# Kernel optimization log

Hardware: AMD Instinct MI355X
Metric: run time of the kernel (lower is better)

Reference implementation:

```python
import jax, jax.numpy as jnp
import numpy as np

B, S, D = 2, 2048, 512
WIN = 64  # local causal window (includes current token)
EPS = 1e-5


def setup_inputs() -> dict:
    key = jax.random.key(0)
    ks = jax.random.split(key, 8)
    sc = 0.02
    return {
        "x":  jax.random.normal(ks[0], (B, S, D), jnp.float32),
        "Wq": jax.random.normal(ks[1], (D, D), jnp.float32) * sc,
        "bq": jnp.zeros((D,), jnp.float32),
        "Wk": jax.random.normal(ks[2], (D, D), jnp.float32) * sc,
        "bk": jnp.zeros((D,), jnp.float32),
        "Wv": jax.random.normal(ks[3], (D, D), jnp.float32) * sc,
        "bv": jnp.zeros((D,), jnp.float32),
        "Wo": jax.random.normal(ks[4], (D, D), jnp.float32) * sc,
        "bo": jnp.zeros((D,), jnp.float32),
        "Wr": jax.random.normal(ks[5], (D, D), jnp.float32) * sc,
        "br": jnp.zeros((D,), jnp.float32),
        "gamma": jnp.ones((D,), jnp.float32),
        "beta":  jnp.zeros((D,), jnp.float32),
    }


def _layernorm(h, gamma, beta):
    mu = jnp.mean(h, axis=-1, keepdims=True)
    var = jnp.mean(jnp.square(h - mu), axis=-1, keepdims=True)
    return (h - mu) * jax.lax.rsqrt(var + EPS) * gamma + beta


def _local_attention(x, Wq, bq, Wk, bk, Wv, bv, Wo, bo):
    q = x @ Wq + bq
    k = x @ Wk + bk
    v = x @ Wv + bv
    kp = jnp.pad(k, ((0, 0), (WIN - 1, 0), (0, 0)))
    vp = jnp.pad(v, ((0, 0), (WIN - 1, 0), (0, 0)))
    idx = jnp.arange(S)[:, None] + jnp.arange(WIN)[None, :]
    kw = kp[:, idx, :]
    vw = vp[:, idx, :]
    scores = jnp.einsum('bsd,bswd->bsw', q, kw) / np.float32(np.sqrt(D))
    valid = (idx >= (WIN - 1 - jnp.zeros((), jnp.int32)))  # padded slots invalid
    valid = idx >= (WIN - 1) - jnp.arange(S)[:, None] * 0
    valid = (idx - (WIN - 1)) >= 0  # key position in original seq >= 0
    scores = jnp.where(valid[None, :, :], scores, jnp.float32(-1e9))
    attn = jax.nn.softmax(scores, axis=-1)
    out = jnp.einsum('bsw,bswd->bsd', attn, vw)
    return out @ Wo + bo


def reference(x, Wq, bq, Wk, bk, Wv, bv, Wo, bo, Wr, br, gamma, beta):
    read = _local_attention(x, Wq, bq, Wk, bk, Wv, bv, Wo, bo)
    sence = x @ Wr + br
    read = _layernorm(read, gamma, beta)
    sence = _layernorm(sence, gamma, beta)
    return jax.nn.gelu(read + sence, approximate=False)
```

## Files before the change

### kernel.cpp

```cpp
#include <hip/hip_runtime.h>
#include <hip/hip_bf16.h>
#include <math.h>

#define BB 2
#define SS 2048
#define DD 512
#define MTOT 4096
#define WINW 64

typedef __attribute__((ext_vector_type(8))) short sv8;
typedef __attribute__((ext_vector_type(4))) float f32x4;

static const size_t OFF_XB   = 0;
static const size_t OFF_WT   = 4194304;
static const size_t OFF_BIAS = 6815744;
static const size_t OFF_Y    = 6823936;
static const size_t OFF_VT   = 23601152;
static const size_t OFF_PP   = 27795456;
static const size_t OFF_ATT  = 0;
static const size_t OFF_READ = 28844032;

static __device__ __forceinline__ float bf2f(short s) {
    unsigned u = ((unsigned)(unsigned short)s) << 16;
    return __builtin_bit_cast(float, u);
}
static __device__ __forceinline__ short f2bf(float f) {
    unsigned u = __builtin_bit_cast(unsigned, f);
    unsigned r = 0x7fffu + ((u >> 16) & 1u);
    u += r;
    return (short)(u >> 16);
}

__global__ __launch_bounds__(256) void cast_x(const float* __restrict__ x,
                                              short* __restrict__ xb, int n4) {
    int i = blockIdx.x * 256 + threadIdx.x;
    if (i < n4) {
        float4 v = ((const float4*)x)[i];
        short4 o;
        o.x = f2bf(v.x); o.y = f2bf(v.y); o.z = f2bf(v.z); o.w = f2bf(v.w);
        ((short4*)xb)[i] = o;
    }
}

__global__ __launch_bounds__(256) void cast_w(const float* __restrict__ Wq,
                                              const float* __restrict__ Wk,
                                              const float* __restrict__ Wv,
                                              const float* __restrict__ Wr,
                                              const float* __restrict__ Wo,
                                              short* __restrict__ wt) {
    __shared__ float tile[32][33];
    int z = blockIdx.z;
    const float* W = (z == 0) ? Wq : (z == 1) ? Wk : (z == 2) ? Wv : (z == 3) ? Wr : Wo;
    int k0 = blockIdx.y * 32, n0 = blockIdx.x * 32;
    int tx = threadIdx.x & 31, ty = threadIdx.x >> 5;
    for (int r = ty; r < 32; r += 8)
        tile[r][tx] = W[(size_t)(k0 + r) * 512 + n0 + tx];
    __syncthreads();
    short* o = wt + (size_t)z * 512 * 512;
    for (int r = ty; r < 32; r += 8)
        o[(size_t)(n0 + r) * 512 + k0 + tx] = f2bf(tile[tx][r]);
}

__global__ __launch_bounds__(256) void prep_bias(const float* __restrict__ bq,
                                                 const float* __restrict__ bk,
                                                 const float* __restrict__ bv,
                                                 const float* __restrict__ br,
                                                 float* __restrict__ ball) {
    int i = blockIdx.x * 256 + threadIdx.x;
    int sel = i >> 9;
    const float* src = (sel == 0) ? bq : (sel == 1) ? bk : (sel == 2) ? bv : br;
    ball[i] = src[i & 511];
}

__global__ __launch_bounds__(256) void gemm_bt(const short* __restrict__ A,
                                               const short* __restrict__ Bt,
                                               const float* __restrict__ bias,
                                               short* __restrict__ Cout, int ldc,
                                               short* __restrict__ vt) {
    const int K = 512;
    const int LDL = 72;
    __shared__ __align__(16) short lA[128 * LDL];
    __shared__ __align__(16) short lB[128 * LDL];
    int tid = threadIdx.x;
    int mbase = blockIdx.y * 128;
    int nbase = blockIdx.x * 128;
    int lane = tid & 63, wave = tid >> 6;
    int wm = wave >> 1, wn = wave & 1;

    f32x4 acc[4][4] = {};

    for (int k0 = 0; k0 < K; k0 += 64) {
#pragma unroll
        for (int t = 0; t < 4; ++t) {
            int c = tid + t * 256;
            int row = c >> 3, slot = c & 7;
            sv8 va = *(const sv8*)(A + (size_t)(mbase + row) * K + k0 + slot * 8);
            *(sv8*)&lA[row * LDL + slot * 8] = va;
            sv8 vb = *(const sv8*)(Bt + (size_t)(nbase + row) * K + k0 + slot * 8);
            *(sv8*)&lB[row * LDL + slot * 8] = vb;
        }
        __syncthreads();
#pragma unroll
        for (int kk = 0; kk < 2; ++kk) {
            int koff = kk * 32 + (lane >> 4) * 8;
            sv8 af[4], bfr[4];
#pragma unroll
            for (int m = 0; m < 4; ++m)
                af[m] = *(const sv8*)&lA[(wm * 64 + m * 16 + (lane & 15)) * LDL + koff];
#pragma unroll
            for (int n = 0; n < 4; ++n)
                bfr[n] = *(const sv8*)&lB[(wn * 64 + n * 16 + (lane & 15)) * LDL + koff];
#pragma unroll
            for (int m = 0; m < 4; ++m)
#pragma unroll
                for (int n = 0; n < 4; ++n)
                    acc[m][n] = __builtin_amdgcn_mfma_f32_16x16x32_bf16(
                        af[m], bfr[n], acc[m][n], 0, 0, 0);
        }
        __syncthreads();
    }

    int r0 = (lane >> 4) * 4, c0 = lane & 15;
    bool tovt = (vt != nullptr) && (nbase >= 1024) && (nbase < 1536);
#pragma unroll
    for (int m = 0; m < 4; ++m) {
#pragma unroll
        for (int n = 0; n < 4; ++n) {
            int col = nbase + wn * 64 + n * 16 + c0;
            float bv = bias[col];
            if (tovt) {
                int d = col - 1024;
                int row0 = mbase + wm * 64 + m * 16 + r0;
                int bb = row0 >> 11, t = row0 & 2047;
                short4 o;
                o.x = f2bf(acc[m][n][0] + bv);
                o.y = f2bf(acc[m][n][1] + bv);
                o.z = f2bf(acc[m][n][2] + bv);
                o.w = f2bf(acc[m][n][3] + bv);
                *(short4*)(vt + (size_t)(bb * 512 + d) * 2048 + t) = o;
            } else {
#pragma unroll
                for (int j = 0; j < 4; ++j) {
                    int row = mbase + wm * 64 + m * 16 + r0 + j;
                    Cout[(size_t)row * ldc + col] = f2bf(acc[m][n][j] + bv);
                }
            }
        }
    }
}

__global__ __launch_bounds__(256) void attn_scores(const short* __restrict__ Y,
                                                   short* __restrict__ Pp) {
    __shared__ float sS[64][132];
    int tile = blockIdx.x;
    int b = tile >> 5;
    int t0 = (tile & 31) * 64;
    int s0 = tile * 64;
    int tid = threadIdx.x, lane = tid & 63, wave = tid >> 6;
    int wm = wave >> 1, wn = wave & 1;

    f32x4 acc[2][4] = {};
    const short* Q = Y;
    const short* Kb = Y + 512;

    int arow[2], brow[4];
#pragma unroll
    for (int m = 0; m < 2; ++m) arow[m] = s0 + wm * 32 + m * 16 + (lane & 15);
#pragma unroll
    for (int n = 0; n < 4; ++n) {
        int kr = t0 - 64 + wn * 64 + n * 16 + (lane & 15);
        if (kr < 0) kr = 0;
        brow[n] = (b << 11) + kr;
    }
#pragma unroll
    for (int step = 0; step < 16; ++step) {
        int koff = step * 32 + (lane >> 4) * 8;
        sv8 af[2], bfr[4];
#pragma unroll
        for (int m = 0; m < 2; ++m)
            af[m] = *(const sv8*)(Q + (size_t)arow[m] * 2048 + koff);
#pragma unroll
        for (int n = 0; n < 4; ++n)
            bfr[n] = *(const sv8*)(Kb + (size_t)brow[n] * 2048 + koff);
#pragma unroll
        for (int m = 0; m < 2; ++m)
#pragma unroll
            for (int n = 0; n < 4; ++n)
                acc[m][n] = __builtin_amdgcn_mfma_f32_16x16x32_bf16(
                    af[m], bfr[n], acc[m][n], 0, 0, 0);
    }
    int r0 = (lane >> 4) * 4, c0 = lane & 15;
#pragma unroll
    for (int m = 0; m < 2; ++m)
#pragma unroll
        for (int n = 0; n < 4; ++n) {
            int jc = wn * 64 + n * 16 + c0;
#pragma unroll
            for (int j = 0; j < 4; ++j)
                sS[wm * 32 + m * 16 + r0 + j][jc] =
                    acc[m][n][j] * 0.04419417382415922f;
        }
    __syncthreads();

    int q = tid >> 2, j0 = (tid & 3) * 32;
    float v[32];
    float mx = -1e30f;
    int jlo = q + 1;
    int jmin0 = 64 - t0;
    if (jmin0 > jlo) jlo = jmin0;
    int jhi = q + 64;
#pragma unroll
    for (int jj = 0; jj < 32; ++jj) {
        int j = j0 + jj;
        bool ok = (j >= jlo) && (j <= jhi);
        float s = ok ? sS[q][j] : -1e30f;
        v[jj] = s;
        mx = fmaxf(mx, s);
    }
    mx = fmaxf(mx, __shfl_xor(mx, 1));
    mx = fmaxf(mx, __shfl_xor(mx, 2));
    float sum = 0.f;
#pragma unroll
    for (int jj = 0; jj < 32; ++jj) {
        float e = (v[jj] > -1e29f) ? __expf(v[jj] - mx) : 0.f;
        v[jj] = e;
        sum += e;
    }
    sum += __shfl_xor(sum, 1);
    sum += __shfl_xor(sum, 2);
    float inv = 1.f / sum;
    short* dst = Pp + (size_t)tile * 8192 + q * 128 + j0;
#pragma unroll
    for (int k = 0; k < 4; ++k) {
        sv8 o;
#pragma unroll
        for (int e = 0; e < 8; ++e) o[e] = f2bf(v[k * 8 + e] * inv);
        *(sv8*)(dst + k * 8) = o;
    }
}

__global__ __launch_bounds__(256) void attn_pv(const short* __restrict__ Pp,
                                               const short* __restrict__ Vt,
                                               short* __restrict__ att) {
    int tile = blockIdx.y, dchunk = blockIdx.x;
    int b = tile >> 5;
    int t0 = (tile & 31) * 64;
    int s0 = tile * 64;
    int tid = threadIdx.x, lane = tid & 63, wave = tid >> 6;
    int wm = wave >> 1, wn = wave & 1;

    f32x4 acc[2][4] = {};
    const short* Pbase = Pp + (size_t)tile * 8192;
#pragma unroll
    for (int ks = 0; ks < 4; ++ks) {
        int koff = ks * 32 + (lane >> 4) * 8;
        sv8 af[2], bfr[4];
#pragma unroll
        for (int m = 0; m < 2; ++m)
            af[m] = *(const sv8*)(Pbase + (wm * 32 + m * 16 + (lane & 15)) * 128 + koff);
#pragma unroll
        for (int n = 0; n < 4; ++n) {
            int d = dchunk * 128 + wn * 64 + n * 16 + (lane & 15);
            long off = (long)(b * 512 + d) * 2048 + (t0 - 64 + koff);
            bfr[n] = *(const sv8*)(Vt + off);
        }
#pragma unroll
        for (int m = 0; m < 2; ++m)
#pragma unroll
            for (int n = 0; n < 4; ++n)
                acc[m][n] = __builtin_amdgcn_mfma_f32_16x16x32_bf16(
                    af[m], bfr[n], acc[m][n], 0, 0, 0);
    }
    int r0 = (lane >> 4) * 4, c0 = lane & 15;
#pragma unroll
    for (int m = 0; m < 2; ++m)
#pragma unroll
        for (int n = 0; n < 4; ++n) {
            int col = dchunk * 128 + wn * 64 + n * 16 + c0;
#pragma unroll
            for (int j = 0; j < 4; ++j) {
                int row = s0 + wm * 32 + m * 16 + r0 + j;
                att[(size_t)row * 512 + col] = f2bf(acc[m][n][j]);
            }
        }
}

__global__ __launch_bounds__(256) void ln_gelu(const short* __restrict__ readb,
                                               const short* __restrict__ Y,
                                               const float* __restrict__ gamma,
                                               const float* __restrict__ beta,
                                               float* __restrict__ out) {
    int s = blockIdx.x;
    int tid = threadIdx.x;
    const short* r = readb + (size_t)s * 512;
    const short* sn = Y + (size_t)s * 2048 + 1536;
    float r0 = bf2f(r[tid]), r1 = bf2f(r[tid + 256]);
    float s0 = bf2f(sn[tid]), s1 = bf2f(sn[tid + 256]);

    float v0 = r0 + r1, v1 = r0 * r0 + r1 * r1;
    float v2 = s0 + s1, v3 = s0 * s0 + s1 * s1;
#pragma unroll
    for (int off = 32; off; off >>= 1) {
        v0 += __shfl_xor(v0, off);
        v1 += __shfl_xor(v1, off);
        v2 += __shfl_xor(v2, off);
        v3 += __shfl_xor(v3, off);
    }
    __shared__ float red[4][4];
    int wave = tid >> 6, lane = tid & 63;
    if (lane == 0) {
        red[wave][0] = v0; red[wave][1] = v1; red[wave][2] = v2; red[wave][3] = v3;
    }
    __syncthreads();
    float t0 = red[0][0] + red[1][0] + red[2][0] + red[3][0];
    float t1 = red[0][1] + red[1][1] + red[2][1] + red[3][1];
    float t2 = red[0][2] + red[1][2] + red[2][2] + red[3][2];
    float t3 = red[0][3] + red[1][3] + red[2][3] + red[3][3];

    float mu_r = t0 * (1.f / 512.f);
    float var_r = t1 * (1.f / 512.f) - mu_r * mu_r;
    float is_r = rsqrtf(var_r + 1e-5f);
    float mu_s = t2 * (1.f / 512.f);
    float var_s = t3 * (1.f / 512.f) - mu_s * mu_s;
    float is_s = rsqrtf(var_s + 1e-5f);

    float g0 = gamma[tid], be0 = beta[tid];
    float g1 = gamma[tid + 256], be1 = beta[tid + 256];
    float x0 = (r0 - mu_r) * is_r * g0 + be0 + (s0 - mu_s) * is_s * g0 + be0;
    float x1 = (r1 - mu_r) * is_r * g1 + be1 + (s1 - mu_s) * is_s * g1 + be1;
    float y0 = 0.5f * x0 * (1.f + erff(x0 * 0.70710678118654752f));
    float y1 = 0.5f * x1 * (1.f + erff(x1 * 0.70710678118654752f));
    out[(size_t)s * 512 + tid] = y0;
    out[(size_t)s * 512 + tid + 256] = y1;
}

extern "C" void kernel_launch(void* const* d_in, const int* in_sizes, int n_in,
                              void* d_out, int out_size, void* d_ws, size_t ws_size,
                              hipStream_t stream) {
    const float* x  = (const float*)d_in[0];
    const float* Wq = (const float*)d_in[1];
    const float* bq = (const float*)d_in[2];
    const float* Wk = (const float*)d_in[3];
    const float* bk = (const float*)d_in[4];
    const float* Wv = (const float*)d_in[5];
    const float* bv = (const float*)d_in[6];
    const float* Wo = (const float*)d_in[7];
    const float* bo = (const float*)d_in[8];
    const float* Wr = (const float*)d_in[9];
    const float* br = (const float*)d_in[10];
    const float* gamma = (const float*)d_in[11];
    const float* beta  = (const float*)d_in[12];

    char* ws = (char*)d_ws;
    short* xb    = (short*)(ws + OFF_XB);
    short* wt    = (short*)(ws + OFF_WT);
    float* ball  = (float*)(ws + OFF_BIAS);
    short* Y     = (short*)(ws + OFF_Y);
    short* vtb   = (short*)(ws + OFF_VT);
    short* Pp    = (short*)(ws + OFF_PP);
    short* att   = (short*)(ws + OFF_ATT);
    short* readb = (short*)(ws + OFF_READ);

    cast_x<<<2048, 256, 0, stream>>>(x, xb, MTOT * DD / 4);
    cast_w<<<dim3(16, 16, 5), 256, 0, stream>>>(Wq, Wk, Wv, Wr, Wo, wt);
    prep_bias<<<8, 256, 0, stream>>>(bq, bk, bv, br, ball);

    gemm_bt<<<dim3(16, 32), 256, 0, stream>>>(xb, wt, ball, Y, 2048, vtb);

    attn_scores<<<64, 256, 0, stream>>>(Y, Pp);
    attn_pv<<<dim3(4, 64), 256, 0, stream>>>(Pp, vtb, att);

    gemm_bt<<<dim3(4, 32), 256, 0, stream>>>(att, wt + (size_t)4 * 512 * 512, bo,
                                             readb, 512, nullptr);

    ln_gelu<<<4096, 256, 0, stream>>>(readb, Y, gamma, beta, (float*)d_out);
}
```

Baseline: 149.5 us.

## Fuse attention scores and PV, split V projection, use direct-to-LDS GEMM loads

Merges the score/softmax kernel with the P·V kernel so probabilities stay in shared memory instead of round-tripping through global memory. The V projection becomes a separate GEMM instance that writes the transposed V layout via swapped MFMA operands, giving contiguous stores. The GEMM tile loads switch to global_load_lds direct-to-LDS transfers with an unpadded LDS layout. Risks include fewer blocks in the fused attention kernel (64) and possible LDS bank conflicts without padding.

Result: slower. 161.5 us (+8.0%).

```diff
diff --git a/kernel.cpp b/kernel.cpp
--- a/kernel.cpp
+++ b/kernel.cpp
@@ -6,7 +6,6 @@
 #define SS 2048
 #define DD 512
 #define MTOT 4096
-#define WINW 64
 
 typedef __attribute__((ext_vector_type(8))) short sv8;
 typedef __attribute__((ext_vector_type(4))) float f32x4;
@@ -15,10 +14,9 @@
 static const size_t OFF_WT   = 4194304;
 static const size_t OFF_BIAS = 6815744;
 static const size_t OFF_Y    = 6823936;
-static const size_t OFF_VT   = 23601152;
-static const size_t OFF_PP   = 27795456;
+static const size_t OFF_VT   = 19406848;
+static const size_t OFF_READ = 23601152;
 static const size_t OFF_ATT  = 0;
-static const size_t OFF_READ = 28844032;
 
 static __device__ __forceinline__ float bf2f(short s) {
     unsigned u = ((unsigned)(unsigned short)s) << 16;
@@ -30,6 +28,11 @@
     u += r;
     return (short)(u >> 16);
 }
+
+#define GLOAD_LDS16(gp, lp)                                                        \
+    __builtin_amdgcn_global_load_lds(                                              \
+        (const __attribute__((address_space(1))) unsigned*)(gp),                   \
+        (__attribute__((address_space(3))) unsigned*)(lp), 16, 0, 0)
 
 __global__ __launch_bounds__(256) void cast_x(const float* __restrict__ x,
                                               short* __restrict__ xb, int n4) {
@@ -44,13 +47,13 @@
 
 __global__ __launch_bounds__(256) void cast_w(const float* __restrict__ Wq,
                                               const float* __restrict__ Wk,
+                                              const float* __restrict__ Wr,
                                               const float* __restrict__ Wv,
-                                              const float* __restrict__ Wr,
                                               const float* __restrict__ Wo,
                                               short* __restrict__ wt) {
     __shared__ float tile[32][33];
     int z = blockIdx.z;
-    const float* W = (z == 0) ? Wq : (z == 1) ? Wk : (z == 2) ? Wv : (z == 3) ? Wr : Wo;
+    const float* W = (z == 0) ? Wq : (z == 1) ? Wk : (z == 2) ? Wr : (z == 3) ? Wv : Wo;
     int k0 = blockIdx.y * 32, n0 = blockIdx.x * 32;
     int tx = threadIdx.x & 31, ty = threadIdx.x >> 5;
     for (int r = ty; r < 32; r += 8)
@@ -63,24 +66,22 @@
 
 __global__ __launch_bounds__(256) void prep_bias(const float* __restrict__ bq,
                                                  const float* __restrict__ bk,
+                                                 const float* __restrict__ br,
                                                  const float* __restrict__ bv,
-                                                 const float* __restrict__ br,
                                                  float* __restrict__ ball) {
     int i = blockIdx.x * 256 + threadIdx.x;
     int sel = i >> 9;
-    const float* src = (sel == 0) ? bq : (sel == 1) ? bk : (sel == 2) ? bv : br;
+    const float* src = (sel == 0) ? bq : (sel == 1) ? bk : (sel == 2) ? br : bv;
     ball[i] = src[i & 511];
 }
 
+template <int MODE>
 __global__ __launch_bounds__(256) void gemm_bt(const short* __restrict__ A,
                                                const short* __restrict__ Bt,
                                                const float* __restrict__ bias,
-                                               short* __restrict__ Cout, int ldc,
-                                               short* __restrict__ vt) {
-    const int K = 512;
-    const int LDL = 72;
-    __shared__ __align__(16) short lA[128 * LDL];
-    __shared__ __align__(16) short lB[128 * LDL];
+                                               short* __restrict__ Cout, int ldc) {
+    __shared__ __align__(16) short lA[128 * 64];
+    __shared__ __align__(16) short lB[128 * 64];
     int tid = threadIdx.x;
     int mbase = blockIdx.y * 128;
     int nbase = blockIdx.x * 128;
@@ -89,15 +90,16 @@
 
     f32x4 acc[4][4] = {};
 
-    for (int k0 = 0; k0 < K; k0 += 64) {
-#pragma unroll
-        for (int t = 0; t < 4; ++t) {
-            int c = tid + t * 256;
-            int row = c >> 3, slot = c & 7;
-            sv8 va = *(const sv8*)(A + (size_t)(mbase + row) * K + k0 + slot * 8);
-            *(sv8*)&lA[row * LDL + slot * 8] = va;
-            sv8 vb = *(const sv8*)(Bt + (size_t)(nbase + row) * K + k0 + slot * 8);
-            *(sv8*)&lB[row * LDL + slot * 8] = vb;
+    int srow = (lane >> 3);
+    int scol = (lane & 7) * 8;
+
+    for (int k0 = 0; k0 < 512; k0 += 64) {
+#pragma unroll
+        for (int c = 0; c < 4; ++c) {
+            int ch = wave * 4 + c;
+            int row = ch * 8 + srow;
+            GLOAD_LDS16(A + (size_t)(mbase + row) * 512 + k0 + scol, &lA[ch * 512]);
+            GLOAD_LDS16(Bt + (size_t)(nbase + row) * 512 + k0 + scol, &lB[ch * 512]);
         }
         __syncthreads();
 #pragma unroll
@@ -106,52 +108,61 @@
             sv8 af[4], bfr[4];
 #pragma unroll
             for (int m = 0; m < 4; ++m)
-                af[m] = *(const sv8*)&lA[(wm * 64 + m * 16 + (lane & 15)) * LDL + koff];
+                af[m] = *(const sv8*)&lA[(wm * 64 + m * 16 + (lane & 15)) * 64 + koff];
 #pragma unroll
             for (int n = 0; n < 4; ++n)
-                bfr[n] = *(const sv8*)&lB[(wn * 64 + n * 16 + (lane & 15)) * LDL + koff];
+                bfr[n] = *(const sv8*)&lB[(wn * 64 + n * 16 + (lane & 15)) * 64 + koff];
 #pragma unroll
             for (int m = 0; m < 4; ++m)
 #pragma unroll
-                for (int n = 0; n < 4; ++n)
-                    acc[m][n] = __builtin_amdgcn_mfma_f32_16x16x32_bf16(
-                        af[m], bfr[n], acc[m][n], 0, 0, 0);
+                for (int n = 0; n < 4; ++n) {
+                    if (MODE == 0)
+                        acc[m][n] = __builtin_amdgcn_mfma_f32_16x16x32_bf16(
+                            af[m], bfr[n], acc[m][n], 0, 0, 0);
+                    else
+                        acc[m][n] = __builtin_amdgcn_mfma_f32_16x16x32_bf16(
+                            bfr[n], af[m], acc[m][n], 0, 0, 0);
+                }
         }
         __syncthreads();
     }
 
     int r0 = (lane >> 4) * 4, c0 = lane & 15;
-    bool tovt = (vt != nullptr) && (nbase >= 1024) && (nbase < 1536);
-#pragma unroll
-    for (int m = 0; m < 4; ++m) {
-#pragma unroll
-        for (int n = 0; n < 4; ++n) {
-            int col = nbase + wn * 64 + n * 16 + c0;
-            float bv = bias[col];
-            if (tovt) {
-                int d = col - 1024;
-                int row0 = mbase + wm * 64 + m * 16 + r0;
-                int bb = row0 >> 11, t = row0 & 2047;
-                short4 o;
-                o.x = f2bf(acc[m][n][0] + bv);
-                o.y = f2bf(acc[m][n][1] + bv);
-                o.z = f2bf(acc[m][n][2] + bv);
-                o.w = f2bf(acc[m][n][3] + bv);
-                *(short4*)(vt + (size_t)(bb * 512 + d) * 2048 + t) = o;
-            } else {
+    if (MODE == 0) {
+#pragma unroll
+        for (int m = 0; m < 4; ++m)
+#pragma unroll
+            for (int n = 0; n < 4; ++n) {
+                int col = nbase + wn * 64 + n * 16 + c0;
+                float bv = bias[col];
 #pragma unroll
                 for (int j = 0; j < 4; ++j) {
                     int row = mbase + wm * 64 + m * 16 + r0 + j;
                     Cout[(size_t)row * ldc + col] = f2bf(acc[m][n][j] + bv);
                 }
             }
-        }
-    }
-}
-
-__global__ __launch_bounds__(256) void attn_scores(const short* __restrict__ Y,
-                                                   short* __restrict__ Pp) {
+    } else {
+        int bb = mbase >> 11, tb = mbase & 2047;
+#pragma unroll
+        for (int m = 0; m < 4; ++m)
+#pragma unroll
+            for (int n = 0; n < 4; ++n) {
+                int dl = nbase + wn * 64 + n * 16 + r0;
+                int tl = tb + wm * 64 + m * 16 + c0;
+#pragma unroll
+                for (int j = 0; j < 4; ++j) {
+                    float v = acc[m][n][j] + bias[dl + j];
+                    Cout[((size_t)bb * 512 + dl + j) * 2048 + tl] = f2bf(v);
+                }
+            }
+    }
+}
+
+__global__ __launch_bounds__(256) void attn_fused(const short* __restrict__ Y,
+                                                  const short* __restrict__ Vt,
+                                                  short* __restrict__ att) {
     __shared__ float sS[64][132];
+    __shared__ __align__(16) short sP[64 * 128];
     int tile = blockIdx.x;
     int b = tile >> 5;
     int t0 = (tile & 31) * 64;
@@ -162,7 +173,6 @@
     f32x4 acc[2][4] = {};
     const short* Q = Y;
     const short* Kb = Y + 512;
-
     int arow[2], brow[4];
 #pragma unroll
     for (int m = 0; m < 2; ++m) arow[m] = s0 + wm * 32 + m * 16 + (lane & 15);
@@ -178,10 +188,10 @@
         sv8 af[2], bfr[4];
 #pragma unroll
         for (int m = 0; m < 2; ++m)
-            af[m] = *(const sv8*)(Q + (size_t)arow[m] * 2048 + koff);
+            af[m] = *(const sv8*)(Q + (size_t)arow[m] * 1536 + koff);
 #pragma unroll
         for (int n = 0; n < 4; ++n)
-            bfr[n] = *(const sv8*)(Kb + (size_t)brow[n] * 2048 + koff);
+            bfr[n] = *(const sv8*)(Kb + (size_t)brow[n] * 1536 + koff);
 #pragma unroll
         for (int m = 0; m < 2; ++m)
 #pragma unroll
@@ -202,85 +212,74 @@
         }
     __syncthreads();
 
-    int q = tid >> 2, j0 = (tid & 3) * 32;
-    float v[32];
-    float mx = -1e30f;
-    int jlo = q + 1;
-    int jmin0 = 64 - t0;
-    if (jmin0 > jlo) jlo = jmin0;
-    int jhi = q + 64;
-#pragma unroll
-    for (int jj = 0; jj < 32; ++jj) {
-        int j = j0 + jj;
-        bool ok = (j >= jlo) && (j <= jhi);
-        float s = ok ? sS[q][j] : -1e30f;
-        v[jj] = s;
-        mx = fmaxf(mx, s);
-    }
-    mx = fmaxf(mx, __shfl_xor(mx, 1));
-    mx = fmaxf(mx, __shfl_xor(mx, 2));
-    float sum = 0.f;
-#pragma unroll
-    for (int jj = 0; jj < 32; ++jj) {
-        float e = (v[jj] > -1e29f) ? __expf(v[jj] - mx) : 0.f;
-        v[jj] = e;
-        sum += e;
-    }
-    sum += __shfl_xor(sum, 1);
-    sum += __shfl_xor(sum, 2);
-    float inv = 1.f / sum;
-    short* dst = Pp + (size_t)tile * 8192 + q * 128 + j0;
-#pragma unroll
-    for (int k = 0; k < 4; ++k) {
-        sv8 o;
-#pragma unroll
-        for (int e = 0; e < 8; ++e) o[e] = f2bf(v[k * 8 + e] * inv);
-        *(sv8*)(dst + k * 8) = o;
-    }
-}
-
-__global__ __launch_bounds__(256) void attn_pv(const short* __restrict__ Pp,
-                                               const short* __restrict__ Vt,
-                                               short* __restrict__ att) {
-    int tile = blockIdx.y, dchunk = blockIdx.x;
-    int b = tile >> 5;
-    int t0 = (tile & 31) * 64;
-    int s0 = tile * 64;
-    int tid = threadIdx.x, lane = tid & 63, wave = tid >> 6;
-    int wm = wave >> 1, wn = wave & 1;
-
-    f32x4 acc[2][4] = {};
-    const short* Pbase = Pp + (size_t)tile * 8192;
+    {
+        int q = tid >> 2, j0 = (tid & 3) * 32;
+        float v[32];
+        float mx = -1e30f;
+        int jlo = q + 1;
+        int jmin0 = 64 - t0;
+        if (jmin0 > jlo) jlo = jmin0;
+        int jhi = q + 64;
+#pragma unroll
+        for (int jj = 0; jj < 32; ++jj) {
+            int j = j0 + jj;
+            bool ok = (j >= jlo) && (j <= jhi);
+            float s = ok ? sS[q][j] : -1e30f;
+            v[jj] = s;
+            mx = fmaxf(mx, s);
+        }
+        mx = fmaxf(mx, __shfl_xor(mx, 1));
+        mx = fmaxf(mx, __shfl_xor(mx, 2));
+        float sum = 0.f;
+#pragma unroll
+        for (int jj = 0; jj < 32; ++jj) {
+            float e = (v[jj] > -1e29f) ? __expf(v[jj] - mx) : 0.f;
+            v[jj] = e;
+            sum += e;
+        }
+        sum += __shfl_xor(sum, 1);
+        sum += __shfl_xor(sum, 2);
+        float inv = 1.f / sum;
+        short* dst = &sP[q * 128 + j0];
+#pragma unroll
+        for (int k = 0; k < 4; ++k) {
+            sv8 o;
+#pragma unroll
+            for (int e = 0; e < 8; ++e) o[e] = f2bf(v[k * 8 + e] * inv);
+            *(sv8*)(dst + k * 8) = o;
+        }
+    }
+    __syncthreads();
+
+    f32x4 acc2[4][8] = {};
+    const short* Vb = Vt + (size_t)b * 512 * 2048;
 #pragma unroll
     for (int ks = 0; ks < 4; ++ks) {
         int koff = ks * 32 + (lane >> 4) * 8;
-        sv8 af[2], bfr[4];
-#pragma unroll
-        for (int m = 0; m < 2; ++m)
-            af[m] = *(const sv8*)(Pbase + (wm * 32 + m * 16 + (lane & 15)) * 128 + koff);
-#pragma unroll
-        for (int n = 0; n < 4; ++n) {
-            int d = dchunk * 128 + wn * 64 + n * 16 + (lane & 15);
-            long off = (long)(b * 512 + d) * 2048 + (t0 - 64 + koff);
-            bfr[n] = *(const sv8*)(Vt + off);
-        }
-#pragma unroll
-        for (int m = 0; m < 2; ++m)
-#pragma unroll
-            for (int n = 0; n < 4; ++n)
-                acc[m][n] = __builtin_amdgcn_mfma_f32_16x16x32_bf16(
-                    af[m], bfr[n], acc[m][n], 0, 0, 0);
-    }
-    int r0 = (lane >> 4) * 4, c0 = lane & 15;
-#pragma unroll
-    for (int m = 0; m < 2; ++m)
-#pragma unroll
-        for (int n = 0; n < 4; ++n) {
-            int col = dchunk * 128 + wn * 64 + n * 16 + c0;
+        sv8 paf[4];
+#pragma unroll
+        for (int m = 0; m < 4; ++m)
+            paf[m] = *(const sv8*)&sP[(m * 16 + (lane & 15)) * 128 + koff];
+#pragma unroll
+        for (int n = 0; n < 8; ++n) {
+            int d = wave * 128 + n * 16 + (lane & 15);
+            long off = (long)d * 2048 + (t0 - 64 + koff);
+            sv8 vv = *(const sv8*)(Vb + off);
+#pragma unroll
+            for (int m = 0; m < 4; ++m)
+                acc2[m][n] = __builtin_amdgcn_mfma_f32_16x16x32_bf16(
+                    paf[m], vv, acc2[m][n], 0, 0, 0);
+        }
+    }
+#pragma unroll
+    for (int m = 0; m < 4; ++m)
+#pragma unroll
+        for (int n = 0; n < 8; ++n) {
+            int col = wave * 128 + n * 16 + c0;
 #pragma unroll
             for (int j = 0; j < 4; ++j) {
-                int row = s0 + wm * 32 + m * 16 + r0 + j;
-                att[(size_t)row * 512 + col] = f2bf(acc[m][n][j]);
+                int row = s0 + m * 16 + r0 + j;
+                att[(size_t)row * 512 + col] = f2bf(acc2[m][n][j]);
             }
         }
 }
@@ -293,7 +292,7 @@
     int s = blockIdx.x;
     int tid = threadIdx.x;
     const short* r = readb + (size_t)s * 512;
-    const short* sn = Y + (size_t)s * 2048 + 1536;
+    const short* sn = Y + (size_t)s * 1536 + 1024;
     float r0 = bf2f(r[tid]), r1 = bf2f(r[tid + 256]);
     float s0 = bf2f(sn[tid]), s1 = bf2f(sn[tid + 256]);
 
@@ -357,21 +356,21 @@
     float* ball  = (float*)(ws + OFF_BIAS);
     short* Y     = (short*)(ws + OFF_Y);
     short* vtb   = (short*)(ws + OFF_VT);
-    short* Pp    = (short*)(ws + OFF_PP);
     short* att   = (short*)(ws + OFF_ATT);
     short* readb = (short*)(ws + OFF_READ);
 
     cast_x<<<2048, 256, 0, stream>>>(x, xb, MTOT * DD / 4);
-    cast_w<<<dim3(16, 16, 5), 256, 0, stream>>>(Wq, Wk, Wv, Wr, Wo, wt);
-    prep_bias<<<8, 256, 0, stream>>>(bq, bk, bv, br, ball);
-
-    gemm_bt<<<dim3(16, 32), 256, 0, stream>>>(xb, wt, ball, Y, 2048, vtb);
-
-    attn_scores<<<64, 256, 0, stream>>>(Y, Pp);
-    attn_pv<<<dim3(4, 64), 256, 0, stream>>>(Pp, vtb, att);
-
-    gemm_bt<<<dim3(4, 32), 256, 0, stream>>>(att, wt + (size_t)4 * 512 * 512, bo,
-                                             readb, 512, nullptr);
+    cast_w<<<dim3(16, 16, 5), 256, 0, stream>>>(Wq, Wk, Wr, Wv, Wo, wt);
+    prep_bias<<<8, 256, 0, stream>>>(bq, bk, br, bv, ball);
+
+    gemm_bt<0><<<dim3(12, 32), 256, 0, stream>>>(xb, wt, ball, Y, 1536);
+    gemm_bt<1><<<dim3(4, 32), 256, 0, stream>>>(xb, wt + (size_t)3 * 512 * 512,
+                                                ball + 1536, vtb, 0);
+
+    attn_fused<<<64, 256, 0, stream>>>(Y, vtb, att);
+
+    gemm_bt<0><<<dim3(4, 32), 256, 0, stream>>>(att, wt + (size_t)4 * 512 * 512, bo,
+                                                readb, 512);
 
     ln_gelu<<<4096, 256, 0, stream>>>(readb, Y, gamma, beta, (float*)d_out);
 }
```

## Use direct global-to-LDS loads in GEMM, compact Y, and coalesce V-transpose stores

Applied to the files above, without the earlier changes.

The GEMM tile loads now use global_load_lds to write 16-byte chunks straight into unpadded shared memory, skipping the register round trip. Y no longer keeps a V region, so its row stride drops from 2048 to 1536 and the sense columns are remapped. V tiles swap the MFMA operands so the transposed store writes contiguous along t. The weight cast and bias prep are merged into one launch. Removing the LDS padding may bring back bank conflicts on the fragment reads.

Result: slower. 157.2 us (+5.2%).

```diff
diff --git a/kernel.cpp b/kernel.cpp
--- a/kernel.cpp
+++ b/kernel.cpp
@@ -6,7 +6,6 @@
 #define SS 2048
 #define DD 512
 #define MTOT 4096
-#define WINW 64
 
 typedef __attribute__((ext_vector_type(8))) short sv8;
 typedef __attribute__((ext_vector_type(4))) float f32x4;
@@ -15,10 +14,10 @@
 static const size_t OFF_WT   = 4194304;
 static const size_t OFF_BIAS = 6815744;
 static const size_t OFF_Y    = 6823936;
-static const size_t OFF_VT   = 23601152;
+static const size_t OFF_VT   = 19406848;
+static const size_t OFF_READ = 23601152;
 static const size_t OFF_PP   = 27795456;
 static const size_t OFF_ATT  = 0;
-static const size_t OFF_READ = 28844032;
 
 static __device__ __forceinline__ float bf2f(short s) {
     unsigned u = ((unsigned)(unsigned short)s) << 16;
@@ -30,6 +29,11 @@
     u += r;
     return (short)(u >> 16);
 }
+
+#define GLOAD_LDS16(gp, lp)                                                        \
+    __builtin_amdgcn_global_load_lds(                                              \
+        (const __attribute__((address_space(1))) unsigned*)(gp),                   \
+        (__attribute__((address_space(3))) unsigned*)(lp), 16, 0, 0)
 
 __global__ __launch_bounds__(256) void cast_x(const float* __restrict__ x,
                                               short* __restrict__ xb, int n4) {
@@ -42,14 +46,27 @@
     }
 }
 
-__global__ __launch_bounds__(256) void cast_w(const float* __restrict__ Wq,
-                                              const float* __restrict__ Wk,
-                                              const float* __restrict__ Wv,
-                                              const float* __restrict__ Wr,
-                                              const float* __restrict__ Wo,
-                                              short* __restrict__ wt) {
+__global__ __launch_bounds__(256) void prep_all(const float* __restrict__ Wq,
+                                                const float* __restrict__ Wk,
+                                                const float* __restrict__ Wv,
+                                                const float* __restrict__ Wr,
+                                                const float* __restrict__ Wo,
+                                                const float* __restrict__ bq,
+                                                const float* __restrict__ bk,
+                                                const float* __restrict__ bv,
+                                                const float* __restrict__ br,
+                                                short* __restrict__ wt,
+                                                float* __restrict__ ball) {
+    int z = blockIdx.z;
+    if (z == 5) {
+        if (blockIdx.y != 0 || blockIdx.x >= 8) return;
+        int i = blockIdx.x * 256 + threadIdx.x;
+        int sel = i >> 9;
+        const float* src = (sel == 0) ? bq : (sel == 1) ? bk : (sel == 2) ? bv : br;
+        ball[i] = src[i & 511];
+        return;
+    }
     __shared__ float tile[32][33];
-    int z = blockIdx.z;
     const float* W = (z == 0) ? Wq : (z == 1) ? Wk : (z == 2) ? Wv : (z == 3) ? Wr : Wo;
     int k0 = blockIdx.y * 32, n0 = blockIdx.x * 32;
     int tx = threadIdx.x & 31, ty = threadIdx.x >> 5;
@@ -61,43 +78,33 @@
         o[(size_t)(n0 + r) * 512 + k0 + tx] = f2bf(tile[tx][r]);
 }
 
-__global__ __launch_bounds__(256) void prep_bias(const float* __restrict__ bq,
-                                                 const float* __restrict__ bk,
-                                                 const float* __restrict__ bv,
-                                                 const float* __restrict__ br,
-                                                 float* __restrict__ ball) {
-    int i = blockIdx.x * 256 + threadIdx.x;
-    int sel = i >> 9;
-    const float* src = (sel == 0) ? bq : (sel == 1) ? bk : (sel == 2) ? bv : br;
-    ball[i] = src[i & 511];
-}
-
+template <int GEMM1>
 __global__ __launch_bounds__(256) void gemm_bt(const short* __restrict__ A,
                                                const short* __restrict__ Bt,
                                                const float* __restrict__ bias,
                                                short* __restrict__ Cout, int ldc,
                                                short* __restrict__ vt) {
-    const int K = 512;
-    const int LDL = 72;
-    __shared__ __align__(16) short lA[128 * LDL];
-    __shared__ __align__(16) short lB[128 * LDL];
+    __shared__ __align__(16) short lA[128 * 64];
+    __shared__ __align__(16) short lB[128 * 64];
     int tid = threadIdx.x;
     int mbase = blockIdx.y * 128;
     int nbase = blockIdx.x * 128;
     int lane = tid & 63, wave = tid >> 6;
     int wm = wave >> 1, wn = wave & 1;
+    bool vswap = GEMM1 && (nbase >= 1024) && (nbase < 1536);
 
     f32x4 acc[4][4] = {};
 
-    for (int k0 = 0; k0 < K; k0 += 64) {
-#pragma unroll
-        for (int t = 0; t < 4; ++t) {
-            int c = tid + t * 256;
-            int row = c >> 3, slot = c & 7;
-            sv8 va = *(const sv8*)(A + (size_t)(mbase + row) * K + k0 + slot * 8);
-            *(sv8*)&lA[row * LDL + slot * 8] = va;
-            sv8 vb = *(const sv8*)(Bt + (size_t)(nbase + row) * K + k0 + slot * 8);
-            *(sv8*)&lB[row * LDL + slot * 8] = vb;
+    int srow = (lane >> 3);
+    int scol = (lane & 7) * 8;
+
+    for (int k0 = 0; k0 < 512; k0 += 64) {
+#pragma unroll
+        for (int c = 0; c < 4; ++c) {
+            int ch = wave * 4 + c;
+            int row = ch * 8 + srow;
+            GLOAD_LDS16(A + (size_t)(mbase + row) * 512 + k0 + scol, &lA[ch * 512]);
+            GLOAD_LDS16(Bt + (size_t)(nbase + row) * 512 + k0 + scol, &lB[ch * 512]);
         }
         __syncthreads();
 #pragma unroll
@@ -106,46 +113,59 @@
             sv8 af[4], bfr[4];
 #pragma unroll
             for (int m = 0; m < 4; ++m)
-                af[m] = *(const sv8*)&lA[(wm * 64 + m * 16 + (lane & 15)) * LDL + koff];
+                af[m] = *(const sv8*)&lA[(wm * 64 + m * 16 + (lane & 15)) * 64 + koff];
 #pragma unroll
             for (int n = 0; n < 4; ++n)
-                bfr[n] = *(const sv8*)&lB[(wn * 64 + n * 16 + (lane & 15)) * LDL + koff];
-#pragma unroll
-            for (int m = 0; m < 4; ++m)
-#pragma unroll
-                for (int n = 0; n < 4; ++n)
-                    acc[m][n] = __builtin_amdgcn_mfma_f32_16x16x32_bf16(
-                        af[m], bfr[n], acc[m][n], 0, 0, 0);
+                bfr[n] = *(const sv8*)&lB[(wn * 64 + n * 16 + (lane & 15)) * 64 + koff];
+            if (!vswap) {
+#pragma unroll
+                for (int m = 0; m < 4; ++m)
+#pragma unroll
+                    for (int n = 0; n < 4; ++n)
+                        acc[m][n] = __builtin_amdgcn_mfma_f32_16x16x32_bf16(
+                            af[m], bfr[n], acc[m][n], 0, 0, 0);
+            } else {
+#pragma unroll
+                for (int m = 0; m < 4; ++m)
+#pragma unroll
+                    for (int n = 0; n < 4; ++n)
+                        acc[m][n] = __builtin_amdgcn_mfma_f32_16x16x32_bf16(
+                            bfr[n], af[m], acc[m][n], 0, 0, 0);
+            }
         }
         __syncthreads();
     }
 
     int r0 = (lane >> 4) * 4, c0 = lane & 15;
-    bool tovt = (vt != nullptr) && (nbase >= 1024) && (nbase < 1536);
-#pragma unroll
-    for (int m = 0; m < 4; ++m) {
-#pragma unroll
-        for (int n = 0; n < 4; ++n) {
-            int col = nbase + wn * 64 + n * 16 + c0;
-            float bv = bias[col];
-            if (tovt) {
-                int d = col - 1024;
-                int row0 = mbase + wm * 64 + m * 16 + r0;
-                int bb = row0 >> 11, t = row0 & 2047;
-                short4 o;
-                o.x = f2bf(acc[m][n][0] + bv);
-                o.y = f2bf(acc[m][n][1] + bv);
-                o.z = f2bf(acc[m][n][2] + bv);
-                o.w = f2bf(acc[m][n][3] + bv);
-                *(short4*)(vt + (size_t)(bb * 512 + d) * 2048 + t) = o;
-            } else {
+    if (!vswap) {
+#pragma unroll
+        for (int m = 0; m < 4; ++m)
+#pragma unroll
+            for (int n = 0; n < 4; ++n) {
+                int col = nbase + wn * 64 + n * 16 + c0;
+                float bv = bias[col];
+                int ycol = (GEMM1 && col >= 1536) ? col - 512 : col;
 #pragma unroll
                 for (int j = 0; j < 4; ++j) {
                     int row = mbase + wm * 64 + m * 16 + r0 + j;
-                    Cout[(size_t)row * ldc + col] = f2bf(acc[m][n][j] + bv);
+                    Cout[(size_t)row * ldc + ycol] = f2bf(acc[m][n][j] + bv);
                 }
             }
-        }
+    } else {
+        int bb = mbase >> 11, tb = mbase & 2047;
+#pragma unroll
+        for (int m = 0; m < 4; ++m)
+#pragma unroll
+            for (int n = 0; n < 4; ++n) {
+                int dglob = nbase + wn * 64 + n * 16 + r0;
+                int d = dglob - 1024;
+                int tl = tb + wm * 64 + m * 16 + c0;
+#pragma unroll
+                for (int j = 0; j < 4; ++j) {
+                    float v = acc[m][n][j] + bias[dglob + j];
+                    vt[((size_t)bb * 512 + d + j) * 2048 + tl] = f2bf(v);
+                }
+            }
     }
 }
 
@@ -178,10 +198,10 @@
         sv8 af[2], bfr[4];
 #pragma unroll
         for (int m = 0; m < 2; ++m)
-            af[m] = *(const sv8*)(Q + (size_t)arow[m] * 2048 + koff);
+            af[m] = *(const sv8*)(Q + (size_t)arow[m] * 1536 + koff);
 #pragma unroll
         for (int n = 0; n < 4; ++n)
-            bfr[n] = *(const sv8*)(Kb + (size_t)brow[n] * 2048 + koff);
+            bfr[n] = *(const sv8*)(Kb + (size_t)brow[n] * 1536 + koff);
 #pragma unroll
         for (int m = 0; m < 2; ++m)
 #pragma unroll
@@ -293,7 +313,7 @@
     int s = blockIdx.x;
     int tid = threadIdx.x;
     const short* r = readb + (size_t)s * 512;
-    const short* sn = Y + (size_t)s * 2048 + 1536;
+    const short* sn = Y + (size_t)s * 1536 + 1024;
     float r0 = bf2f(r[tid]), r1 = bf2f(r[tid + 256]);
     float s0 = bf2f(sn[tid]), s1 = bf2f(sn[tid + 256]);
 
@@ -357,21 +377,21 @@
     float* ball  = (float*)(ws + OFF_BIAS);
     short* Y     = (short*)(ws + OFF_Y);
     short* vtb   = (short*)(ws + OFF_VT);
+    short* readb = (short*)(ws + OFF_READ);
     short* Pp    = (short*)(ws + OFF_PP);
     short* att   = (short*)(ws + OFF_ATT);
-    short* readb = (short*)(ws + OFF_READ);
 
     cast_x<<<2048, 256, 0, stream>>>(x, xb, MTOT * DD / 4);
-    cast_w<<<dim3(16, 16, 5), 256, 0, stream>>>(Wq, Wk, Wv, Wr, Wo, wt);
-    prep_bias<<<8, 256, 0, stream>>>(bq, bk, bv, br, ball);
-
-    gemm_bt<<<dim3(16, 32), 256, 0, stream>>>(xb, wt, ball, Y, 2048, vtb);
+    prep_all<<<dim3(16, 16, 6), 256, 0, stream>>>(Wq, Wk, Wv, Wr, Wo, bq, bk, bv, br,
+                                                  wt, ball);
+
+    gemm_bt<1><<<dim3(16, 32), 256, 0, stream>>>(xb, wt, ball, Y, 1536, vtb);
 
     attn_scores<<<64, 256, 0, stream>>>(Y, Pp);
     attn_pv<<<dim3(4, 64), 256, 0, stream>>>(Pp, vtb, att);
 
-    gemm_bt<<<dim3(4, 32), 256, 0, stream>>>(att, wt + (size_t)4 * 512 * 512, bo,
-                                             readb, 512, nullptr);
+    gemm_bt<0><<<dim3(4, 32), 256, 0, stream>>>(att, wt + (size_t)4 * 512 * 512, bo,
+                                                readb, 512, nullptr);
 
     ln_gelu<<<4096, 256, 0, stream>>>(readb, Y, gamma, beta, (float*)d_out);
 }
```
